# Optimization experiments

Measured on AMD Instinct MI355X. Metric: run time of the kernel, lower is better.

The kernel has to match this reference:

```python
import jax, jax.numpy as jnp
import numpy as np

D_MODEL = 1024
D_FF = 4096
N_EXPERTS = 8
TOP_K = 2

def setup_inputs() -> dict:
    key = jax.random.key(0)
    ks = jax.random.split(key, 8)
    s = 0.02
    return {
        "x": jax.random.normal(ks[0], (4, 2048, D_MODEL), dtype=jnp.float32),
        "W1": jax.random.normal(ks[1], (N_EXPERTS, D_MODEL, D_FF), dtype=jnp.float32) * s,
        "b1": jnp.zeros((N_EXPERTS, D_FF), dtype=jnp.float32),
        "W2": jax.random.normal(ks[2], (N_EXPERTS, D_FF, D_MODEL), dtype=jnp.float32) * s,
        "b2": jnp.zeros((N_EXPERTS, D_MODEL), dtype=jnp.float32),
        "Wg": jax.random.normal(ks[3], (D_MODEL, N_EXPERTS), dtype=jnp.float32) * s,
        "bg": jnp.zeros((N_EXPERTS,), dtype=jnp.float32),
    }

def reference(x, W1, b1, W2, b2, Wg, bg):
    B, S, D = x.shape
    # Gating network
    gate_logits = jnp.einsum('bsd,de->bse', x, Wg) + bg
    gate_probs = jax.nn.softmax(gate_logits, axis=-1)  # (B,S,E)
    # Top-k routing on softmax probs (matches torch.topk(F.softmax(logits)))
    top_k_probs, top_k_indices = jax.lax.top_k(gate_probs, TOP_K)  # (B,S,k)
    T = B * S
    x_flat = x.reshape(T, D)
    idx_flat = top_k_indices.reshape(T, TOP_K)
    prob_flat = top_k_probs.reshape(T, TOP_K)
    # Per-token combine weight for each expert: sum of top-k probs routed to it
    # combine[t, e] = sum_j prob_flat[t, j] * (idx_flat[t, j] == e)
    onehot = jax.nn.one_hot(idx_flat, N_EXPERTS, dtype=x.dtype)  # (T,k,E)
    combine = jnp.einsum('tk,tke->te', prob_flat, onehot)  # (T,E)
    out = jnp.zeros((T, D), dtype=x.dtype)
    for e in range(N_EXPERTS):  # static small loop over experts
        h = jax.nn.relu(x_flat @ W1[e] + b1[e])  # (T, d_ff)
        y = h @ W2[e] + b2[e]                    # (T, d_model)
        out = out + combine[:, e:e+1] * y
    return out.reshape(B, S, D), gate_probs
```

## Files before the change

kernel.cpp:

```cpp
#include <hip/hip_runtime.h>

#define D_MODEL 1024
#define D_FF    4096
#define N_EXP   8
#define BM 128
#define BN 128
#define BK 64

typedef __attribute__((ext_vector_type(8))) short bf16x8;
typedef __attribute__((ext_vector_type(4))) float f32x4;
typedef unsigned int u32;

__device__ __forceinline__ unsigned short f2bf(float f) {
  union { float f; unsigned u; } v; v.f = f;
  unsigned r = v.u + 0x7FFFu + ((v.u >> 16) & 1u);
  return (unsigned short)(r >> 16);
}

__device__ __forceinline__ void gl_lds16(const void* g, void* l) {
  __builtin_amdgcn_global_load_lds((const __attribute__((address_space(1))) u32*)g,
                                   (__attribute__((address_space(3))) u32*)l, 16, 0, 0);
}

__global__ __launch_bounds__(256)
void transpose_convert_kernel(const float* __restrict__ src, unsigned short* __restrict__ dst,
                              int Ksub, int Nsrc, int k0, int n0, int Nchunk,
                              unsigned long long eStride) {
  __shared__ u32 s32k[32][65];
  int e = blockIdx.z;
  int kb = blockIdx.x * 64, nb = blockIdx.y * 64;
  const float* se = src + (size_t)e * eStride + (size_t)(k0 + kb) * Nsrc + (n0 + nb);
  unsigned short* de = dst + (size_t)e * Nchunk * Ksub + (size_t)nb * Ksub + kb;
  int tid = threadIdx.x;
  int kh = tid >> 4;
  int n4 = (tid & 15) * 4;
  #pragma unroll
  for (int p = 0; p < 2; p++) {
    int k = kh * 2 + p * 32;
    float4 v0 = *(const float4*)(se + (size_t)k * Nsrc + n4);
    float4 v1 = *(const float4*)(se + (size_t)(k + 1) * Nsrc + n4);
    #pragma unroll
    for (int j = 0; j < 4; j++) {
      u32 pk = (u32)f2bf(((const float*)&v0)[j]) |
               ((u32)f2bf(((const float*)&v1)[j]) << 16);
      s32k[k >> 1][n4 + j] = pk;
    }
  }
  __syncthreads();
  #pragma unroll
  for (int c = 0; c < 2; c++) {
    int id = tid + c * 256;
    int n = id >> 3, kc = id & 7;
    uint4 o;
    o.x = s32k[kc * 4 + 0][n];
    o.y = s32k[kc * 4 + 1][n];
    o.z = s32k[kc * 4 + 2][n];
    o.w = s32k[kc * 4 + 3][n];
    *(uint4*)(de + (size_t)n * Ksub + kc * 8) = o;
  }
}

__global__ void gating_kernel(const float* __restrict__ x,
                              const float* __restrict__ Wg,
                              const float* __restrict__ bg,
                              float* __restrict__ gate_out,
                              unsigned short* __restrict__ xb,
                              int* __restrict__ cnt,
                              int* __restrict__ tokIdx,
                              float* __restrict__ tokW, int T) {
  int wv = threadIdx.x >> 6, lane = threadIdx.x & 63;
  int t = blockIdx.x * 4 + wv;
  if (t >= T) return;
  const float* xr = x + (size_t)t * D_MODEL + lane * 16;
  float acc[N_EXP];
  #pragma unroll
  for (int e = 0; e < N_EXP; e++) acc[e] = 0.f;
  ushort4 xc[4];
  #pragma unroll
  for (int q = 0; q < 4; q++) {
    float4 xv = *(const float4*)(xr + q * 4);
    xc[q].x = f2bf(xv.x); xc[q].y = f2bf(xv.y);
    xc[q].z = f2bf(xv.z); xc[q].w = f2bf(xv.w);
    #pragma unroll
    for (int r = 0; r < 4; r++) {
      float xs = ((const float*)&xv)[r];
      const float* wrow = Wg + (size_t)(lane * 16 + q * 4 + r) * N_EXP;
      float4 wa = *(const float4*)wrow;
      float4 wb = *(const float4*)(wrow + 4);
      acc[0] += xs * wa.x; acc[1] += xs * wa.y; acc[2] += xs * wa.z; acc[3] += xs * wa.w;
      acc[4] += xs * wb.x; acc[5] += xs * wb.y; acc[6] += xs * wb.z; acc[7] += xs * wb.w;
    }
  }
  unsigned short* xbr = xb + (size_t)t * D_MODEL + lane * 16;
  #pragma unroll
  for (int q = 0; q < 4; q++) *(ushort4*)(xbr + q * 4) = xc[q];
  #pragma unroll
  for (int off = 32; off > 0; off >>= 1) {
    #pragma unroll
    for (int e = 0; e < N_EXP; e++) acc[e] += __shfl_xor(acc[e], off);
  }
  if (lane == 0) {
    float l[N_EXP], p[N_EXP];
    float m = -1e30f;
    #pragma unroll
    for (int e = 0; e < N_EXP; e++) { l[e] = acc[e] + bg[e]; m = fmaxf(m, l[e]); }
    float s = 0.f;
    #pragma unroll
    for (int e = 0; e < N_EXP; e++) { p[e] = __expf(l[e] - m); s += p[e]; }
    float inv = 1.f / s;
    #pragma unroll
    for (int e = 0; e < N_EXP; e++) { p[e] *= inv; gate_out[(size_t)t * N_EXP + e] = p[e]; }
    int e1 = 0;
    #pragma unroll
    for (int e = 1; e < N_EXP; e++) if (p[e] > p[e1]) e1 = e;
    int e2 = (e1 == 0) ? 1 : 0;
    #pragma unroll
    for (int e = 0; e < N_EXP; e++) if (e != e1 && p[e] > p[e2]) e2 = e;
    int pos = atomicAdd(cnt + e1, 1);
    tokIdx[(size_t)e1 * T + pos] = t; tokW[(size_t)e1 * T + pos] = p[e1];
    pos = atomicAdd(cnt + e2, 1);
    tokIdx[(size_t)e2 * T + pos] = t; tokW[(size_t)e2 * T + pos] = p[e2];
  }
}

__global__ void schedule_kernel(const int* __restrict__ cnt, int* __restrict__ meta,
                                int* __restrict__ tE, int* __restrict__ tB,
                                int* __restrict__ tV, int T, int maxTiles) {
  if (threadIdx.x != 0 || blockIdx.x != 0) return;
  int t = 0;
  for (int e = 0; e < N_EXP; e++) {
    int c = cnt[e];
    for (int r = 0; r < c && t < maxTiles; r += BM) {
      tE[t] = e; tB[t] = e * T + r; tV[t] = min(BM, c - r); t++;
    }
  }
  meta[0] = t;
}

__global__ __launch_bounds__(256)
void gemm1_kernel(const unsigned short* __restrict__ xb,
                  const unsigned short* __restrict__ w1t,
                  const float* __restrict__ b1,
                  const int* __restrict__ meta,
                  const int* __restrict__ tE, const int* __restrict__ tB,
                  const int* __restrict__ tV, const int* __restrict__ tokIdx,
                  unsigned short* __restrict__ h, int FFC, int chunk_off, int ncolLog2) {
  __shared__ unsigned short As[BM * BK];
  __shared__ unsigned short Bs[BN * BK];
  __shared__ int stok[BM];

  int total = gridDim.x;
  int L = blockIdx.x;
  int q = total >> 3, r8 = total & 7;
  int xcd = L & 7, idx = L >> 3;
  int work = (xcd < r8) ? (xcd * (q + 1) + idx) : (r8 * (q + 1) + (xcd - r8) * q + idx);
  int ncol = 1 << ncolLog2;
  int tile = work >> ncolLog2;
  int cb = work & (ncol - 1);
  if (tile >= meta[0]) return;
  int e = tE[tile], base = tB[tile], valid = tV[tile];
  int tid = threadIdx.x;

  if (tid < BM) stok[tid] = tokIdx[base + (tid < valid ? tid : valid - 1)];
  __syncthreads();

  int w = tid >> 6, lane = tid & 63;
  int lr = lane >> 3, lc = lane & 7;

  const unsigned short* panel = w1t + (size_t)e * FFC * D_MODEL;
  const unsigned short* aBase[4];
  const unsigned short* bBase[4];
  #pragma unroll
  for (int p = 0; p < 4; p++) {
    int row = (w * 4 + p) * 8 + lr;
    int cA = (lc - row) & 7;
    aBase[p] = xb + (size_t)stok[row] * D_MODEL + cA * 8;
    int cB = (lc - row) & 7;
    bBase[p] = panel + (size_t)(cb * BN + row) * D_MODEL + cB * 8;
  }

  int wr = w >> 1, wc = w & 1;
  int l15 = lane & 15, l4 = lane >> 4;
  int aOff[2][4], bOff[2][4];
  #pragma unroll
  for (int kk = 0; kk < 2; kk++) {
    #pragma unroll
    for (int m = 0; m < 4; m++) {
      int row = wr * 64 + m * 16 + l15;
      int c = kk * 4 + l4;
      aOff[kk][m] = row * 64 + (((c + row) & 7) << 3);
      int col = wc * 64 + m * 16 + l15;
      bOff[kk][m] = col * 64 + (((c + col) & 7) << 3);
    }
  }

  f32x4 acc[4][4];
  #pragma unroll
  for (int m = 0; m < 4; m++)
    #pragma unroll
    for (int n = 0; n < 4; n++) acc[m][n] = (f32x4){0.f, 0.f, 0.f, 0.f};

  for (int kt = 0; kt < D_MODEL / BK; kt++) {
    #pragma unroll
    for (int p = 0; p < 4; p++)
      gl_lds16(aBase[p] + kt * BK, &As[(w * 4 + p) * 512]);
    #pragma unroll
    for (int p = 0; p < 4; p++)
      gl_lds16(bBase[p] + kt * BK, &Bs[(w * 4 + p) * 512]);
    __syncthreads();
    #pragma unroll
    for (int kk = 0; kk < 2; kk++) {
      bf16x8 a[4], b[4];
      #pragma unroll
      for (int m = 0; m < 4; m++) a[m] = *(const bf16x8*)&As[aOff[kk][m]];
      #pragma unroll
      for (int n = 0; n < 4; n++) b[n] = *(const bf16x8*)&Bs[bOff[kk][n]];
      #pragma unroll
      for (int m = 0; m < 4; m++)
        #pragma unroll
        for (int n = 0; n < 4; n++)
          acc[m][n] = __builtin_amdgcn_mfma_f32_16x16x32_bf16(a[m], b[n], acc[m][n], 0, 0, 0);
    }
    __syncthreads();
  }

  #pragma unroll
  for (int n = 0; n < 4; n++) {
    int colc = cb * BN + wc * 64 + n * 16 + l15;
    float bias = b1[(size_t)e * D_FF + chunk_off + colc];
    #pragma unroll
    for (int m = 0; m < 4; m++) {
      #pragma unroll
      for (int r = 0; r < 4; r++) {
        int row = wr * 64 + m * 16 + l4 * 4 + r;
        float v = acc[m][n][r] + bias;
        v = v > 0.f ? v : 0.f;
        h[(size_t)(tile * BM + row) * FFC + colc] = f2bf(v);
      }
    }
  }
}

__global__ __launch_bounds__(256)
void gemm2_kernel(const unsigned short* __restrict__ h,
                  const unsigned short* __restrict__ w2t,
                  const float* __restrict__ b2,
                  const int* __restrict__ meta,
                  const int* __restrict__ tE, const int* __restrict__ tB,
                  const int* __restrict__ tV, const int* __restrict__ tokIdx,
                  const float* __restrict__ tokW,
                  float* __restrict__ out, int FFC, int chunk_off) {
  __shared__ unsigned short As[BM * BK];
  __shared__ unsigned short Bs[BN * BK];
  __shared__ int stok[BM];
  __shared__ float sw[BM];

  int total = gridDim.x;
  int L = blockIdx.x;
  int q = total >> 3, r8 = total & 7;
  int xcd = L & 7, idx = L >> 3;
  int work = (xcd < r8) ? (xcd * (q + 1) + idx) : (r8 * (q + 1) + (xcd - r8) * q + idx);
  int tile = work >> 4;
  int cb = (work >> 1) & 7;
  int ks = work & 1;
  if (tile >= meta[0]) return;
  int e = tE[tile], base = tB[tile], valid = tV[tile];
  int tid = threadIdx.x;

  if (tid < BM) {
    int rr = tid < valid ? tid : valid - 1;
    stok[tid] = tokIdx[base + rr];
    sw[tid] = tokW[base + rr];
  }
  __syncthreads();

  int w = tid >> 6, lane = tid & 63;
  int lr = lane >> 3, lc = lane & 7;

  const int KT = FFC / BK / 2;
  const int ksOff = ks * KT * BK;

  const unsigned short* panel = w2t + (size_t)e * D_MODEL * FFC;
  const unsigned short* aBase[4];
  const unsigned short* bBase[4];
  #pragma unroll
  for (int p = 0; p < 4; p++) {
    int row = (w * 4 + p) * 8 + lr;
    int cA = (lc - row) & 7;
    aBase[p] = h + (size_t)(tile * BM + row) * FFC + ksOff + cA * 8;
    int cB = (lc - row) & 7;
    bBase[p] = panel + (size_t)(cb * BN + row) * FFC + ksOff + cB * 8;
  }

  int wr = w >> 1, wc = w & 1;
  int l15 = lane & 15, l4 = lane >> 4;
  int aOff[2][4], bOff[2][4];
  #pragma unroll
  for (int kk = 0; kk < 2; kk++) {
    #pragma unroll
    for (int m = 0; m < 4; m++) {
      int row = wr * 64 + m * 16 + l15;
      int c = kk * 4 + l4;
      aOff[kk][m] = row * 64 + (((c + row) & 7) << 3);
      int col = wc * 64 + m * 16 + l15;
      bOff[kk][m] = col * 64 + (((c + col) & 7) << 3);
    }
  }

  f32x4 acc[4][4];
  #pragma unroll
  for (int m = 0; m < 4; m++)
    #pragma unroll
    for (int n = 0; n < 4; n++) acc[m][n] = (f32x4){0.f, 0.f, 0.f, 0.f};

  for (int kt = 0; kt < KT; kt++) {
    #pragma unroll
    for (int p = 0; p < 4; p++)
      gl_lds16(aBase[p] + kt * BK, &As[(w * 4 + p) * 512]);
    #pragma unroll
    for (int p = 0; p < 4; p++)
      gl_lds16(bBase[p] + kt * BK, &Bs[(w * 4 + p) * 512]);
    __syncthreads();
    #pragma unroll
    for (int kk = 0; kk < 2; kk++) {
      bf16x8 a[4], b[4];
      #pragma unroll
      for (int m = 0; m < 4; m++) a[m] = *(const bf16x8*)&As[aOff[kk][m]];
      #pragma unroll
      for (int n = 0; n < 4; n++) b[n] = *(const bf16x8*)&Bs[bOff[kk][n]];
      #pragma unroll
      for (int m = 0; m < 4; m++)
        #pragma unroll
        for (int n = 0; n < 4; n++)
          acc[m][n] = __builtin_amdgcn_mfma_f32_16x16x32_bf16(a[m], b[n], acc[m][n], 0, 0, 0);
    }
    __syncthreads();
  }

  int addBias = (chunk_off == 0 && ks == 0) ? 1 : 0;
  #pragma unroll
  for (int n = 0; n < 4; n++) {
    int colg = cb * BN + wc * 64 + n * 16 + l15;
    float bias = addBias ? b2[(size_t)e * D_MODEL + colg] : 0.f;
    #pragma unroll
    for (int m = 0; m < 4; m++) {
      #pragma unroll
      for (int r = 0; r < 4; r++) {
        int row = wr * 64 + m * 16 + l4 * 4 + r;
        if (row < valid) {
          float v = (acc[m][n][r] + bias) * sw[row];
          atomicAdd(out + (size_t)stok[row] * D_MODEL + colg, v);
        }
      }
    }
  }
}

extern "C" void kernel_launch(void* const* d_in, const int* in_sizes, int n_in,
                              void* d_out, int out_size, void* d_ws, size_t ws_size,
                              hipStream_t stream) {
  const float* x  = (const float*)d_in[0];
  const float* W1 = (const float*)d_in[1];
  const float* b1 = (const float*)d_in[2];
  const float* W2 = (const float*)d_in[3];
  const float* b2 = (const float*)d_in[4];
  const float* Wg = (const float*)d_in[5];
  const float* bg = (const float*)d_in[6];

  int T = in_sizes[0] / D_MODEL;
  float* out = (float*)d_out;
  float* gate_out = out + (size_t)T * D_MODEL;

  char* ws = (char*)d_ws;
  int* cnt  = (int*)(ws + 0);
  int* meta = (int*)(ws + 64);
  int* tE   = (int*)(ws + 128);
  int* tB   = (int*)(ws + 1024);
  int* tV   = (int*)(ws + 2048);
  size_t off = 4096;
  int* tokIdx = (int*)(ws + off);   off += (size_t)N_EXP * T * 4;
  float* tokW = (float*)(ws + off); off += (size_t)N_EXP * T * 4;
  unsigned short* xb = (unsigned short*)(ws + off); off += (size_t)T * D_MODEL * 2;
  off = (off + 255) & ~(size_t)255;

  int maxTiles = (2 * T) / BM + N_EXP;
  int FFC = D_FF;
  while (FFC > 256 &&
         off + (size_t)FFC * (16384 + 16384 + (size_t)maxTiles * BM * 2) > ws_size)
    FFC >>= 1;

  unsigned short* w1t = (unsigned short*)(ws + off); off += (size_t)FFC * 16384;
  unsigned short* w2t = (unsigned short*)(ws + off); off += (size_t)FFC * 16384;
  unsigned short* h   = (unsigned short*)(ws + off);

  hipMemsetAsync(d_out, 0, (size_t)T * D_MODEL * sizeof(float), stream);
  hipMemsetAsync(cnt, 0, N_EXP * sizeof(int), stream);

  gating_kernel<<<(T + 3) / 4, 256, 0, stream>>>(x, Wg, bg, gate_out, xb, cnt, tokIdx, tokW, T);
  schedule_kernel<<<1, 64, 0, stream>>>(cnt, meta, tE, tB, tV, T, maxTiles);

  int ncol1 = FFC / BN;
  int ncol1Log2 = __builtin_ctz(ncol1);
  for (int c = 0; c * FFC < D_FF; c++) {
    transpose_convert_kernel<<<dim3(D_MODEL / 64, FFC / 64, N_EXP), 256, 0, stream>>>(
        W1, w1t, D_MODEL, D_FF, 0, c * FFC, FFC, (unsigned long long)D_MODEL * D_FF);
    transpose_convert_kernel<<<dim3(FFC / 64, D_MODEL / 64, N_EXP), 256, 0, stream>>>(
        W2, w2t, FFC, D_MODEL, c * FFC, 0, D_MODEL, (unsigned long long)D_FF * D_MODEL);
    gemm1_kernel<<<maxTiles * ncol1, 256, 0, stream>>>(
        xb, w1t, b1, meta, tE, tB, tV, tokIdx, h, FFC, c * FFC, ncol1Log2);
    gemm2_kernel<<<maxTiles * (D_MODEL / BN) * 2, 256, 0, stream>>>(
        h, w2t, b2, meta, tE, tB, tV, tokIdx, tokW, out, FFC, c * FFC);
  }
}
```

Baseline: 791.9 us.

## Drop split-K in gemm2, remove shared token staging, raise occupancy hint

Removes the 2-way split-K in the second expert GEMM, so each block covers the full K range and issues half as many atomic adds to the output. It also drops the shared-memory staging of token indices and weights (and the barrier that went with it), reading them directly from global memory. Both GEMMs gain a launch_bounds occupancy hint of 5 blocks per CU. The trade-off is half as many gemm2 blocks with longer K loops, plus possibly extra register pressure or spills from the occupancy cap.

```diff
diff --git a/kernel.cpp b/kernel.cpp
--- a/kernel.cpp
+++ b/kernel.cpp
@@ -137,7 +137,7 @@
   meta[0] = t;
 }
 
-__global__ __launch_bounds__(256)
+__global__ __launch_bounds__(256, 5)
 void gemm1_kernel(const unsigned short* __restrict__ xb,
                   const unsigned short* __restrict__ w1t,
                   const float* __restrict__ b1,
@@ -147,7 +147,6 @@
                   unsigned short* __restrict__ h, int FFC, int chunk_off, int ncolLog2) {
   __shared__ unsigned short As[BM * BK];
   __shared__ unsigned short Bs[BN * BK];
-  __shared__ int stok[BM];
 
   int total = gridDim.x;
   int L = blockIdx.x;
@@ -161,9 +160,6 @@
   int e = tE[tile], base = tB[tile], valid = tV[tile];
   int tid = threadIdx.x;
 
-  if (tid < BM) stok[tid] = tokIdx[base + (tid < valid ? tid : valid - 1)];
-  __syncthreads();
-
   int w = tid >> 6, lane = tid & 63;
   int lr = lane >> 3, lc = lane & 7;
 
@@ -173,10 +169,10 @@
   #pragma unroll
   for (int p = 0; p < 4; p++) {
     int row = (w * 4 + p) * 8 + lr;
+    int tok = tokIdx[base + (row < valid ? row : valid - 1)];
     int cA = (lc - row) & 7;
-    aBase[p] = xb + (size_t)stok[row] * D_MODEL + cA * 8;
-    int cB = (lc - row) & 7;
-    bBase[p] = panel + (size_t)(cb * BN + row) * D_MODEL + cB * 8;
+    aBase[p] = xb + (size_t)tok * D_MODEL + cA * 8;
+    bBase[p] = panel + (size_t)(cb * BN + row) * D_MODEL + cA * 8;
   }
 
   int wr = w >> 1, wc = w & 1;
@@ -241,7 +237,7 @@
   }
 }
 
-__global__ __launch_bounds__(256)
+__global__ __launch_bounds__(256, 5)
 void gemm2_kernel(const unsigned short* __restrict__ h,
                   const unsigned short* __restrict__ w2t,
                   const float* __restrict__ b2,
@@ -252,33 +248,20 @@
                   float* __restrict__ out, int FFC, int chunk_off) {
   __shared__ unsigned short As[BM * BK];
   __shared__ unsigned short Bs[BN * BK];
-  __shared__ int stok[BM];
-  __shared__ float sw[BM];
 
   int total = gridDim.x;
   int L = blockIdx.x;
   int q = total >> 3, r8 = total & 7;
   int xcd = L & 7, idx = L >> 3;
   int work = (xcd < r8) ? (xcd * (q + 1) + idx) : (r8 * (q + 1) + (xcd - r8) * q + idx);
-  int tile = work >> 4;
-  int cb = (work >> 1) & 7;
-  int ks = work & 1;
+  int tile = work >> 3;
+  int cb = work & 7;
   if (tile >= meta[0]) return;
   int e = tE[tile], base = tB[tile], valid = tV[tile];
   int tid = threadIdx.x;
 
-  if (tid < BM) {
-    int rr = tid < valid ? tid : valid - 1;
-    stok[tid] = tokIdx[base + rr];
-    sw[tid] = tokW[base + rr];
-  }
-  __syncthreads();
-
   int w = tid >> 6, lane = tid & 63;
   int lr = lane >> 3, lc = lane & 7;
-
-  const int KT = FFC / BK / 2;
-  const int ksOff = ks * KT * BK;
 
   const unsigned short* panel = w2t + (size_t)e * D_MODEL * FFC;
   const unsigned short* aBase[4];
@@ -287,9 +270,8 @@
   for (int p = 0; p < 4; p++) {
     int row = (w * 4 + p) * 8 + lr;
     int cA = (lc - row) & 7;
-    aBase[p] = h + (size_t)(tile * BM + row) * FFC + ksOff + cA * 8;
-    int cB = (lc - row) & 7;
-    bBase[p] = panel + (size_t)(cb * BN + row) * FFC + ksOff + cB * 8;
+    aBase[p] = h + (size_t)(tile * BM + row) * FFC + cA * 8;
+    bBase[p] = panel + (size_t)(cb * BN + row) * FFC + cA * 8;
   }
 
   int wr = w >> 1, wc = w & 1;
@@ -313,6 +295,7 @@
     #pragma unroll
     for (int n = 0; n < 4; n++) acc[m][n] = (f32x4){0.f, 0.f, 0.f, 0.f};
 
+  int KT = FFC / BK;
   for (int kt = 0; kt < KT; kt++) {
     #pragma unroll
     for (int p = 0; p < 4; p++)
@@ -337,7 +320,7 @@
     __syncthreads();
   }
 
-  int addBias = (chunk_off == 0 && ks == 0) ? 1 : 0;
+  int addBias = (chunk_off == 0) ? 1 : 0;
   #pragma unroll
   for (int n = 0; n < 4; n++) {
     int colg = cb * BN + wc * 64 + n * 16 + l15;
@@ -348,8 +331,10 @@
       for (int r = 0; r < 4; r++) {
         int row = wr * 64 + m * 16 + l4 * 4 + r;
         if (row < valid) {
-          float v = (acc[m][n][r] + bias) * sw[row];
-          atomicAdd(out + (size_t)stok[row] * D_MODEL + colg, v);
+          int tok = tokIdx[base + row];
+          float wgt = tokW[base + row];
+          float v = (acc[m][n][r] + bias) * wgt;
+          atomicAdd(out + (size_t)tok * D_MODEL + colg, v);
         }
       }
     }
@@ -408,7 +393,7 @@
         W2, w2t, FFC, D_MODEL, c * FFC, 0, D_MODEL, (unsigned long long)D_FF * D_MODEL);
     gemm1_kernel<<<maxTiles * ncol1, 256, 0, stream>>>(
         xb, w1t, b1, meta, tE, tB, tV, tokIdx, h, FFC, c * FFC, ncol1Log2);
-    gemm2_kernel<<<maxTiles * (D_MODEL / BN) * 2, 256, 0, stream>>>(
+    gemm2_kernel<<<maxTiles * (D_MODEL / BN), 256, 0, stream>>>(
         h, w2t, b2, meta, tE, tB, tV, tokIdx, tokW, out, FFC, c * FFC);
   }
 }
```

Result: slower. 1.041 ms (+31.5%).
